# Kernel tuning notes

Measured on AMD Instinct MI355X. Metric: run time of the kernel, lower is better.

## Reference

```python
import jax, jax.numpy as jnp
import numpy as np

N = 100_000          # nodes
E = 1_600_000        # edges (avg degree 16)
IN_C, OUT_C = 256, 128


def setup_inputs() -> dict:
    key = jax.random.key(0)
    k1, k2, k3, k4, k5 = jax.random.split(key, 5)
    X = jax.random.normal(k1, (N, IN_C), dtype=jnp.float32)
    # nn.Linear(in, out, bias=False) weight has shape [out, in]
    W = jax.random.normal(k2, (OUT_C, IN_C), dtype=jnp.float32) * (1.0 / np.sqrt(IN_C))
    A_rows = jnp.sort(jax.random.randint(k3, (E,), 0, N, dtype=jnp.int32))
    A_cols = jax.random.randint(k4, (E,), 0, N, dtype=jnp.int32)
    # positive values mimicking symmetric-normalized adjacency entries
    A_vals = jax.random.uniform(k5, (E,), dtype=jnp.float32) * (1.0 / 16.0)
    return {"X": X, "W": W, "A_rows": A_rows, "A_cols": A_cols, "A_vals": A_vals}


def reference(X, W, A_rows, A_cols, A_vals):
    # X = self._linear(X)  ->  X @ W^T   [N, OUT_C]
    H = jnp.einsum("ni,oi->no", X, W)
    # X = torch.sparse.mm(A_hat, X): out[r] += v * H[c] for each edge (r, c, v)
    msgs = A_vals[:, None] * H[A_cols]                      # [E, OUT_C]
    out = jax.ops.segment_sum(msgs, A_rows, num_segments=N)  # [N, OUT_C]
    return out
```

## Files before the change

kernel.cpp:

```cpp
#include <hip/hip_runtime.h>
#include <hip/hip_bf16.h>

#define NNODES 100000
#define NEDGES 1600000
#define IN_C   256
#define OUT_C  128

typedef short bf16x8 __attribute__((ext_vector_type(8)));
typedef float f32x4  __attribute__((ext_vector_type(4)));

static __device__ __forceinline__ unsigned short f2bf(float f) {
    union { float f; unsigned u; } c; c.f = f;
    unsigned r = c.u + 0x7fffu + ((c.u >> 16) & 1u);
    return (unsigned short)(r >> 16);
}

union BF8 { bf16x8 v; unsigned short s[8]; };

__global__ __launch_bounds__(512, 4) void gemm_xwt(const float* __restrict__ X,
                                                   const float* __restrict__ W,
                                                   signed char* __restrict__ H8,
                                                   float* __restrict__ scale) {
    __shared__ unsigned short Wsh[128 * 256];

    const int tid  = threadIdx.x;
    const int lane = tid & 63;
    const int wid  = tid >> 6;

#pragma unroll
    for (int p = 0; p < 16; ++p) {
        int idx = p * 512 + tid;
        int n   = idx >> 6;
        int c4  = idx & 63;
        float4 v = *(const float4*)(W + (size_t)n * IN_C + c4 * 4);
        int byte = (n * 512 + c4 * 8) ^ ((n & 7) << 4);
        *(ushort4*)((char*)Wsh + byte) =
            make_ushort4(f2bf(v.x), f2bf(v.y), f2bf(v.z), f2bf(v.w));
    }
    __syncthreads();

    const int r0   = blockIdx.x * 128 + wid * 16;
    int arow = r0 + (lane & 15);
    if (arow > NNODES - 1) arow = NNODES - 1;
    const float* xrow = X + (size_t)arow * IN_C + (lane >> 4) * 8;

    f32x4 acc[8] = {};
#pragma unroll
    for (int ks = 0; ks < 8; ++ks) {
        float4 a0 = *(const float4*)(xrow + ks * 32);
        float4 a1 = *(const float4*)(xrow + ks * 32 + 4);
        BF8 t;
        t.s[0] = f2bf(a0.x); t.s[1] = f2bf(a0.y); t.s[2] = f2bf(a0.z); t.s[3] = f2bf(a0.w);
        t.s[4] = f2bf(a1.x); t.s[5] = f2bf(a1.y); t.s[6] = f2bf(a1.z); t.s[7] = f2bf(a1.w);
        const int kb = ks * 64 + (lane >> 4) * 16;
#pragma unroll
        for (int n8 = 0; n8 < 8; ++n8) {
            int nr   = n8 * 16 + (lane & 15);
            int byte = (nr * 512 + kb) ^ ((nr & 7) << 4);
            bf16x8 b = *(const bf16x8*)((const char*)Wsh + byte);
            acc[n8] = __builtin_amdgcn_mfma_f32_16x16x32_bf16(t.v, b, acc[n8],
                                                              0, 0, 0);
        }
    }

    float amax[4];
#pragma unroll
    for (int r = 0; r < 4; ++r) {
        float m = 0.f;
#pragma unroll
        for (int n8 = 0; n8 < 8; ++n8) m = fmaxf(m, fabsf(acc[n8][r]));
        amax[r] = m;
    }
#pragma unroll
    for (int d = 1; d < 16; d <<= 1)
#pragma unroll
        for (int r = 0; r < 4; ++r)
            amax[r] = fmaxf(amax[r], __shfl_xor(amax[r], d));

#pragma unroll
    for (int r = 0; r < 4; ++r) {
        int grow = r0 + (lane >> 4) * 4 + r;
        if (grow < NNODES) {
            float am  = amax[r];
            float inv = am > 0.f ? 127.f / am : 0.f;
            if ((lane & 15) == 0) scale[grow] = am * (1.f / 127.f);
#pragma unroll
            for (int n8 = 0; n8 < 8; ++n8) {
                float q = rintf(acc[n8][r] * inv);
                q = fminf(127.f, fmaxf(-127.f, q));
                H8[(size_t)grow * OUT_C + n8 * 16 + (lane & 15)] = (signed char)q;
            }
        }
    }
}

__global__ __launch_bounds__(256) void build_rowptr(const int* __restrict__ rows,
                                                    int* __restrict__ rowptr) {
    int r = blockIdx.x * 256 + threadIdx.x;
    if (r > NNODES) return;
    int lo = 0, hi = NEDGES;
    while (lo < hi) {
        int mid = (lo + hi) >> 1;
        if (rows[mid] < r) lo = mid + 1; else hi = mid;
    }
    rowptr[r] = lo;
}

static __device__ __forceinline__ void edge4(float acc[8], int ec, float ev,
                                             int jg, const uint2* __restrict__ H2,
                                             int cg) {
    int   c = __shfl(ec, jg);
    float v = __shfl(ev, jg);
    uint2 u = H2[(size_t)c * 16 + cg];
    acc[0] += v * (float)(signed char)(u.x);
    acc[1] += v * (float)(signed char)(u.x >> 8);
    acc[2] += v * (float)(signed char)(u.x >> 16);
    acc[3] += v * (float)(signed char)(u.x >> 24);
    acc[4] += v * (float)(signed char)(u.y);
    acc[5] += v * (float)(signed char)(u.y >> 8);
    acc[6] += v * (float)(signed char)(u.y >> 16);
    acc[7] += v * (float)(signed char)(u.y >> 24);
}

__global__ __launch_bounds__(256) void spmm_rows(const uint2* __restrict__ H2,
                                                 const int* __restrict__ rowptr,
                                                 const int* __restrict__ cols,
                                                 const float* __restrict__ vals,
                                                 const float* __restrict__ scale,
                                                 float* __restrict__ out) {
    const int wid  = threadIdx.x >> 6;
    const int lane = threadIdx.x & 63;
    const int g    = lane >> 4;
    const int cg   = lane & 15;

    const int rowA = (blockIdx.x * 4 + wid) * 2;
    const int sA = rowptr[rowA];
    const int eA = rowptr[rowA + 1];
    const int eB = rowptr[rowA + 2];

    float accA[8], accB[8];
#pragma unroll
    for (int t = 0; t < 8; ++t) { accA[t] = 0.f; accB[t] = 0.f; }

    int baseA = sA, baseB = eA;
    while (baseA < eA || baseB < eB) {
        int cntA = eA - baseA; cntA = cntA < 0 ? 0 : (cntA > 64 ? 64 : cntA);
        int cntB = eB - baseB; cntB = cntB < 0 ? 0 : (cntB > 64 ? 64 : cntB);

        int   ecA = 0, ecB = 0;
        float evA = 0.f, evB = 0.f;
        if (lane < cntA) { ecA = cols[baseA + lane]; evA = vals[baseA + lane] * scale[ecA]; }
        if (lane < cntB) { ecB = cols[baseB + lane]; evB = vals[baseB + lane] * scale[ecB]; }

        const int mx = cntA > cntB ? cntA : cntB;
        for (int j = 0; j < mx; j += 8) {
            if (j < cntA)     edge4(accA, ecA, evA, j + g,     H2, cg);
            if (j < cntB)     edge4(accB, ecB, evB, j + g,     H2, cg);
            if (j + 4 < cntA) edge4(accA, ecA, evA, j + 4 + g, H2, cg);
            if (j + 4 < cntB) edge4(accB, ecB, evB, j + 4 + g, H2, cg);
        }

        baseA += cntA;
        baseB += cntB;
    }

#pragma unroll
    for (int t = 0; t < 8; ++t) {
        accA[t] += __shfl_xor(accA[t], 16);
        accA[t] += __shfl_xor(accA[t], 32);
        accB[t] += __shfl_xor(accB[t], 16);
        accB[t] += __shfl_xor(accB[t], 32);
    }
    if (lane < 16) {
        f32x4 a0 = { accA[0], accA[1], accA[2], accA[3] };
        f32x4 a1 = { accA[4], accA[5], accA[6], accA[7] };
        f32x4 b0 = { accB[0], accB[1], accB[2], accB[3] };
        f32x4 b1 = { accB[4], accB[5], accB[6], accB[7] };
        __builtin_nontemporal_store(a0, (f32x4*)(out + (size_t)rowA * OUT_C + cg * 8));
        __builtin_nontemporal_store(a1, (f32x4*)(out + (size_t)rowA * OUT_C + cg * 8 + 4));
        __builtin_nontemporal_store(b0, (f32x4*)(out + (size_t)(rowA + 1) * OUT_C + cg * 8));
        __builtin_nontemporal_store(b1, (f32x4*)(out + (size_t)(rowA + 1) * OUT_C + cg * 8 + 4));
    }
}

extern "C" void kernel_launch(void* const* d_in, const int* in_sizes, int n_in,
                              void* d_out, int out_size, void* d_ws, size_t ws_size,
                              hipStream_t stream) {
    const float* X      = (const float*)d_in[0];
    const float* W      = (const float*)d_in[1];
    const int*   A_rows = (const int*)d_in[2];
    const int*   A_cols = (const int*)d_in[3];
    const float* A_vals = (const float*)d_in[4];
    float* out = (float*)d_out;

    signed char* H8    = (signed char*)d_ws;
    float*       scale = (float*)((char*)d_ws + (size_t)NNODES * OUT_C);
    int*         rowptr = (int*)((char*)scale + (size_t)NNODES * sizeof(float));

    gemm_xwt<<<(NNODES + 127) / 128, 512, 0, stream>>>(X, W, H8, scale);
    build_rowptr<<<(NNODES + 1 + 255) / 256, 256, 0, stream>>>(A_rows, rowptr);
    spmm_rows<<<(NNODES + 7) / 8, 256, 0, stream>>>((const uint2*)H8, rowptr,
                                                    A_cols, A_vals, scale, out);
}
```

Baseline: 91.87 us.

## Store H as offset uint8 and batch gathered loads ahead of FMAs

Quantized H is now stored as unsigned bytes with a +128 offset, so unpacking uses a plain byte-to-float conversion without sign extension. The offset is removed by tracking the per-row sum of edge weights and subtracting 128 times that sum at the end. The SpMM inner loop now handles 16 edges per step and issues all eight gathered loads before the FMAs, giving more memory-level parallelism. The cost is more live registers and extra float error from subtracting a large bias term.

```diff
diff --git a/kernel.cpp b/kernel.cpp
--- a/kernel.cpp
+++ b/kernel.cpp
@@ -19,7 +19,7 @@
 
 __global__ __launch_bounds__(512, 4) void gemm_xwt(const float* __restrict__ X,
                                                    const float* __restrict__ W,
-                                                   signed char* __restrict__ H8,
+                                                   unsigned char* __restrict__ H8,
                                                    float* __restrict__ scale) {
     __shared__ unsigned short Wsh[128 * 256];
 
@@ -88,7 +88,8 @@
             for (int n8 = 0; n8 < 8; ++n8) {
                 float q = rintf(acc[n8][r] * inv);
                 q = fminf(127.f, fmaxf(-127.f, q));
-                H8[(size_t)grow * OUT_C + n8 * 16 + (lane & 15)] = (signed char)q;
+                H8[(size_t)grow * OUT_C + n8 * 16 + (lane & 15)] =
+                    (unsigned char)((int)q + 128);
             }
         }
     }
@@ -106,20 +107,17 @@
     rowptr[r] = lo;
 }
 
-static __device__ __forceinline__ void edge4(float acc[8], int ec, float ev,
-                                             int jg, const uint2* __restrict__ H2,
-                                             int cg) {
-    int   c = __shfl(ec, jg);
-    float v = __shfl(ev, jg);
-    uint2 u = H2[(size_t)c * 16 + cg];
-    acc[0] += v * (float)(signed char)(u.x);
-    acc[1] += v * (float)(signed char)(u.x >> 8);
-    acc[2] += v * (float)(signed char)(u.x >> 16);
-    acc[3] += v * (float)(signed char)(u.x >> 24);
-    acc[4] += v * (float)(signed char)(u.y);
-    acc[5] += v * (float)(signed char)(u.y >> 8);
-    acc[6] += v * (float)(signed char)(u.y >> 16);
-    acc[7] += v * (float)(signed char)(u.y >> 24);
+static __device__ __forceinline__ void fma8(float acc[8], float* sw,
+                                            uint2 u, float v) {
+    *sw += v;
+    acc[0] += v * (float)( u.x        & 0xffu);
+    acc[1] += v * (float)((u.x >>  8) & 0xffu);
+    acc[2] += v * (float)((u.x >> 16) & 0xffu);
+    acc[3] += v * (float)( u.x >> 24);
+    acc[4] += v * (float)( u.y        & 0xffu);
+    acc[5] += v * (float)((u.y >>  8) & 0xffu);
+    acc[6] += v * (float)((u.y >> 16) & 0xffu);
+    acc[7] += v * (float)( u.y >> 24);
 }
 
 __global__ __launch_bounds__(256) void spmm_rows(const uint2* __restrict__ H2,
@@ -141,6 +139,7 @@
     float accA[8], accB[8];
 #pragma unroll
     for (int t = 0; t < 8; ++t) { accA[t] = 0.f; accB[t] = 0.f; }
+    float swA = 0.f, swB = 0.f;
 
     int baseA = sA, baseB = eA;
     while (baseA < eA || baseB < eB) {
@@ -153,11 +152,34 @@
         if (lane < cntB) { ecB = cols[baseB + lane]; evB = vals[baseB + lane] * scale[ecB]; }
 
         const int mx = cntA > cntB ? cntA : cntB;
-        for (int j = 0; j < mx; j += 8) {
-            if (j < cntA)     edge4(accA, ecA, evA, j + g,     H2, cg);
-            if (j < cntB)     edge4(accB, ecB, evB, j + g,     H2, cg);
-            if (j + 4 < cntA) edge4(accA, ecA, evA, j + 4 + g, H2, cg);
-            if (j + 4 < cntB) edge4(accB, ecB, evB, j + 4 + g, H2, cg);
+        for (int j = 0; j < mx; j += 16) {
+            const bool dA0 = j      < cntA, dA1 = j +  4 < cntA,
+                       dA2 = j + 8  < cntA, dA3 = j + 12 < cntA;
+            const bool dB0 = j      < cntB, dB1 = j +  4 < cntB,
+                       dB2 = j + 8  < cntB, dB3 = j + 12 < cntB;
+
+            int cA0 = __shfl(ecA, j + g),      cB0 = __shfl(ecB, j + g);
+            int cA1 = __shfl(ecA, j + 4 + g),  cB1 = __shfl(ecB, j + 4 + g);
+            int cA2 = __shfl(ecA, j + 8 + g),  cB2 = __shfl(ecB, j + 8 + g);
+            int cA3 = __shfl(ecA, j + 12 + g), cB3 = __shfl(ecB, j + 12 + g);
+            uint2 uA0, uA1, uA2, uA3, uB0, uB1, uB2, uB3;
+            if (dA0) uA0 = H2[(size_t)cA0 * 16 + cg];
+            if (dB0) uB0 = H2[(size_t)cB0 * 16 + cg];
+            if (dA1) uA1 = H2[(size_t)cA1 * 16 + cg];
+            if (dB1) uB1 = H2[(size_t)cB1 * 16 + cg];
+            if (dA2) uA2 = H2[(size_t)cA2 * 16 + cg];
+            if (dB2) uB2 = H2[(size_t)cB2 * 16 + cg];
+            if (dA3) uA3 = H2[(size_t)cA3 * 16 + cg];
+            if (dB3) uB3 = H2[(size_t)cB3 * 16 + cg];
+
+            if (dA0) fma8(accA, &swA, uA0, __shfl(evA, j + g));
+            if (dB0) fma8(accB, &swB, uB0, __shfl(evB, j + g));
+            if (dA1) fma8(accA, &swA, uA1, __shfl(evA, j + 4 + g));
+            if (dB1) fma8(accB, &swB, uB1, __shfl(evB, j + 4 + g));
+            if (dA2) fma8(accA, &swA, uA2, __shfl(evA, j + 8 + g));
+            if (dB2) fma8(accB, &swB, uB2, __shfl(evB, j + 8 + g));
+            if (dA3) fma8(accA, &swA, uA3, __shfl(evA, j + 12 + g));
+            if (dB3) fma8(accB, &swB, uB3, __shfl(evB, j + 12 + g));
         }
 
         baseA += cntA;
@@ -171,11 +193,15 @@
         accB[t] += __shfl_xor(accB[t], 16);
         accB[t] += __shfl_xor(accB[t], 32);
     }
+    swA += __shfl_xor(swA, 16); swA += __shfl_xor(swA, 32);
+    swB += __shfl_xor(swB, 16); swB += __shfl_xor(swB, 32);
+
     if (lane < 16) {
-        f32x4 a0 = { accA[0], accA[1], accA[2], accA[3] };
-        f32x4 a1 = { accA[4], accA[5], accA[6], accA[7] };
-        f32x4 b0 = { accB[0], accB[1], accB[2], accB[3] };
-        f32x4 b1 = { accB[4], accB[5], accB[6], accB[7] };
+        const float bA = 128.f * swA, bB = 128.f * swB;
+        f32x4 a0 = { accA[0] - bA, accA[1] - bA, accA[2] - bA, accA[3] - bA };
+        f32x4 a1 = { accA[4] - bA, accA[5] - bA, accA[6] - bA, accA[7] - bA };
+        f32x4 b0 = { accB[0] - bB, accB[1] - bB, accB[2] - bB, accB[3] - bB };
+        f32x4 b1 = { accB[4] - bB, accB[5] - bB, accB[6] - bB, accB[7] - bB };
         __builtin_nontemporal_store(a0, (f32x4*)(out + (size_t)rowA * OUT_C + cg * 8));
         __builtin_nontemporal_store(a1, (f32x4*)(out + (size_t)rowA * OUT_C + cg * 8 + 4));
         __builtin_nontemporal_store(b0, (f32x4*)(out + (size_t)(rowA + 1) * OUT_C + cg * 8));
@@ -193,9 +219,9 @@
     const float* A_vals = (const float*)d_in[4];
     float* out = (float*)d_out;
 
-    signed char* H8    = (signed char*)d_ws;
-    float*       scale = (float*)((char*)d_ws + (size_t)NNODES * OUT_C);
-    int*         rowptr = (int*)((char*)scale + (size_t)NNODES * sizeof(float));
+    unsigned char* H8    = (unsigned char*)d_ws;
+    float*         scale = (float*)((char*)d_ws + (size_t)NNODES * OUT_C);
+    int*           rowptr = (int*)((char*)scale + (size_t)NNODES * sizeof(float));
 
     gemm_xwt<<<(NNODES + 127) / 128, 512, 0, stream>>>(X, W, H8, scale);
     build_rowptr<<<(NNODES + 1 + 255) / 256, 256, 0, stream>>>(A_rows, rowptr);
```

Result: slower. 94.86 us (+3.2%).

## Store H as biased uint8 and gather 16 bytes per lane in SpMM

Applied to the files above, without the earlier changes.

The GEMM now writes quantized H as unsigned bytes offset by 128. The SpMM converts them with plain unsigned byte extracts instead of sign-extending, and removes the bias at the end by subtracting 128 times the sum of edge weights. Each lane now loads a uint4 (16 channels) instead of a uint2, and all gathers in an iteration are issued before the FMAs to increase memory-level parallelism. In exchange each lane holds twice as many accumulators, the reduction gains an extra shuffle stage, and subtracting the bias may cost a little fp32 accuracy.

```diff
diff --git a/kernel.cpp b/kernel.cpp
--- a/kernel.cpp
+++ b/kernel.cpp
@@ -19,7 +19,7 @@
 
 __global__ __launch_bounds__(512, 4) void gemm_xwt(const float* __restrict__ X,
                                                    const float* __restrict__ W,
-                                                   signed char* __restrict__ H8,
+                                                   unsigned char* __restrict__ H8,
                                                    float* __restrict__ scale) {
     __shared__ unsigned short Wsh[128 * 256];
 
@@ -88,7 +88,8 @@
             for (int n8 = 0; n8 < 8; ++n8) {
                 float q = rintf(acc[n8][r] * inv);
                 q = fminf(127.f, fmaxf(-127.f, q));
-                H8[(size_t)grow * OUT_C + n8 * 16 + (lane & 15)] = (signed char)q;
+                H8[(size_t)grow * OUT_C + n8 * 16 + (lane & 15)] =
+                    (unsigned char)((int)q + 128);
             }
         }
     }
@@ -106,23 +107,20 @@
     rowptr[r] = lo;
 }
 
-static __device__ __forceinline__ void edge4(float acc[8], int ec, float ev,
-                                             int jg, const uint2* __restrict__ H2,
-                                             int cg) {
-    int   c = __shfl(ec, jg);
-    float v = __shfl(ev, jg);
-    uint2 u = H2[(size_t)c * 16 + cg];
-    acc[0] += v * (float)(signed char)(u.x);
-    acc[1] += v * (float)(signed char)(u.x >> 8);
-    acc[2] += v * (float)(signed char)(u.x >> 16);
-    acc[3] += v * (float)(signed char)(u.x >> 24);
-    acc[4] += v * (float)(signed char)(u.y);
-    acc[5] += v * (float)(signed char)(u.y >> 8);
-    acc[6] += v * (float)(signed char)(u.y >> 16);
-    acc[7] += v * (float)(signed char)(u.y >> 24);
-}
-
-__global__ __launch_bounds__(256) void spmm_rows(const uint2* __restrict__ H2,
+static __device__ __forceinline__ void fma16(float acc[16], float* sw,
+                                             uint4 u, float v) {
+    *sw += v;
+#pragma unroll
+    for (int d = 0; d < 4; ++d) {
+        unsigned ud = (&u.x)[d];
+        acc[d * 4 + 0] += v * (float)( ud        & 0xffu);
+        acc[d * 4 + 1] += v * (float)((ud >>  8) & 0xffu);
+        acc[d * 4 + 2] += v * (float)((ud >> 16) & 0xffu);
+        acc[d * 4 + 3] += v * (float)( ud >> 24);
+    }
+}
+
+__global__ __launch_bounds__(256) void spmm_rows(const uint4* __restrict__ H4,
                                                  const int* __restrict__ rowptr,
                                                  const int* __restrict__ cols,
                                                  const float* __restrict__ vals,
@@ -130,17 +128,18 @@
                                                  float* __restrict__ out) {
     const int wid  = threadIdx.x >> 6;
     const int lane = threadIdx.x & 63;
-    const int g    = lane >> 4;
-    const int cg   = lane & 15;
+    const int g    = lane >> 3;
+    const int cg   = lane & 7;
 
     const int rowA = (blockIdx.x * 4 + wid) * 2;
     const int sA = rowptr[rowA];
     const int eA = rowptr[rowA + 1];
     const int eB = rowptr[rowA + 2];
 
-    float accA[8], accB[8];
-#pragma unroll
-    for (int t = 0; t < 8; ++t) { accA[t] = 0.f; accB[t] = 0.f; }
+    float accA[16], accB[16];
+#pragma unroll
+    for (int t = 0; t < 16; ++t) { accA[t] = 0.f; accB[t] = 0.f; }
+    float swA = 0.f, swB = 0.f;
 
     int baseA = sA, baseB = eA;
     while (baseA < eA || baseB < eB) {
@@ -153,11 +152,24 @@
         if (lane < cntB) { ecB = cols[baseB + lane]; evB = vals[baseB + lane] * scale[ecB]; }
 
         const int mx = cntA > cntB ? cntA : cntB;
-        for (int j = 0; j < mx; j += 8) {
-            if (j < cntA)     edge4(accA, ecA, evA, j + g,     H2, cg);
-            if (j < cntB)     edge4(accB, ecB, evB, j + g,     H2, cg);
-            if (j + 4 < cntA) edge4(accA, ecA, evA, j + 4 + g, H2, cg);
-            if (j + 4 < cntB) edge4(accB, ecB, evB, j + 4 + g, H2, cg);
+        for (int j = 0; j < mx; j += 16) {
+            const bool dA0 = j < cntA, dA1 = j + 8 < cntA;
+            const bool dB0 = j < cntB, dB1 = j + 8 < cntB;
+
+            uint4 uA0, uA1, uB0, uB1;
+            float vA0, vA1, vB0, vB1;
+            if (dA0) { int c = __shfl(ecA, j + g);     vA0 = __shfl(evA, j + g);
+                       uA0 = H4[(size_t)c * 8 + cg]; }
+            if (dB0) { int c = __shfl(ecB, j + g);     vB0 = __shfl(evB, j + g);
+                       uB0 = H4[(size_t)c * 8 + cg]; }
+            if (dA1) { int c = __shfl(ecA, j + 8 + g); vA1 = __shfl(evA, j + 8 + g);
+                       uA1 = H4[(size_t)c * 8 + cg]; }
+            if (dB1) { int c = __shfl(ecB, j + 8 + g); vB1 = __shfl(evB, j + 8 + g);
+                       uB1 = H4[(size_t)c * 8 + cg]; }
+            if (dA0) fma16(accA, &swA, uA0, vA0);
+            if (dB0) fma16(accB, &swB, uB0, vB0);
+            if (dA1) fma16(accA, &swA, uA1, vA1);
+            if (dB1) fma16(accB, &swB, uB1, vB1);
         }
 
         baseA += cntA;
@@ -165,21 +177,30 @@
     }
 
 #pragma unroll
-    for (int t = 0; t < 8; ++t) {
+    for (int t = 0; t < 16; ++t) {
+        accA[t] += __shfl_xor(accA[t], 8);
         accA[t] += __shfl_xor(accA[t], 16);
         accA[t] += __shfl_xor(accA[t], 32);
+        accB[t] += __shfl_xor(accB[t], 8);
         accB[t] += __shfl_xor(accB[t], 16);
         accB[t] += __shfl_xor(accB[t], 32);
     }
-    if (lane < 16) {
-        f32x4 a0 = { accA[0], accA[1], accA[2], accA[3] };
-        f32x4 a1 = { accA[4], accA[5], accA[6], accA[7] };
-        f32x4 b0 = { accB[0], accB[1], accB[2], accB[3] };
-        f32x4 b1 = { accB[4], accB[5], accB[6], accB[7] };
-        __builtin_nontemporal_store(a0, (f32x4*)(out + (size_t)rowA * OUT_C + cg * 8));
-        __builtin_nontemporal_store(a1, (f32x4*)(out + (size_t)rowA * OUT_C + cg * 8 + 4));
-        __builtin_nontemporal_store(b0, (f32x4*)(out + (size_t)(rowA + 1) * OUT_C + cg * 8));
-        __builtin_nontemporal_store(b1, (f32x4*)(out + (size_t)(rowA + 1) * OUT_C + cg * 8 + 4));
+    swA += __shfl_xor(swA, 8); swA += __shfl_xor(swA, 16); swA += __shfl_xor(swA, 32);
+    swB += __shfl_xor(swB, 8); swB += __shfl_xor(swB, 16); swB += __shfl_xor(swB, 32);
+
+    if (lane < 8) {
+        const float bA = 128.f * swA, bB = 128.f * swB;
+        float* oA = out + (size_t)rowA * OUT_C + cg * 16;
+        float* oB = out + (size_t)(rowA + 1) * OUT_C + cg * 16;
+#pragma unroll
+        for (int q = 0; q < 4; ++q) {
+            f32x4 va = { accA[q * 4 + 0] - bA, accA[q * 4 + 1] - bA,
+                         accA[q * 4 + 2] - bA, accA[q * 4 + 3] - bA };
+            f32x4 vb = { accB[q * 4 + 0] - bB, accB[q * 4 + 1] - bB,
+                         accB[q * 4 + 2] - bB, accB[q * 4 + 3] - bB };
+            __builtin_nontemporal_store(va, (f32x4*)(oA + q * 4));
+            __builtin_nontemporal_store(vb, (f32x4*)(oB + q * 4));
+        }
     }
 }
 
@@ -193,12 +214,12 @@
     const float* A_vals = (const float*)d_in[4];
     float* out = (float*)d_out;
 
-    signed char* H8    = (signed char*)d_ws;
-    float*       scale = (float*)((char*)d_ws + (size_t)NNODES * OUT_C);
-    int*         rowptr = (int*)((char*)scale + (size_t)NNODES * sizeof(float));
+    unsigned char* H8    = (unsigned char*)d_ws;
+    float*         scale = (float*)((char*)d_ws + (size_t)NNODES * OUT_C);
+    int*           rowptr = (int*)((char*)scale + (size_t)NNODES * sizeof(float));
 
     gemm_xwt<<<(NNODES + 127) / 128, 512, 0, stream>>>(X, W, H8, scale);
     build_rowptr<<<(NNODES + 1 + 255) / 256, 256, 0, stream>>>(A_rows, rowptr);
-    spmm_rows<<<(NNODES + 7) / 8, 256, 0, stream>>>((const uint2*)H8, rowptr,
+    spmm_rows<<<(NNODES + 7) / 8, 256, 0, stream>>>((const uint4*)H8, rowptr,
                                                     A_cols, A_vals, scale, out);
 }
```

Measured after the change: 105.9 us. +15.2%, slower.

## Use offset-binary int8 H, nontemporal gathers, and persistent grid-stride SpMM

Applied to the files above, without the earlier changes.

The int8 features are now stored offset by 128 as unsigned bytes, so the SpMM can unpack them with masks and shifts instead of sign extension, and it removes the bias afterwards using a per-row running sum of edge weights. The H gathers switch to nontemporal loads. The SpMM launches a fixed grid of 2048 blocks that stride over row pairs instead of one wave per row pair. Together these aim to trim unpack ALU work and launch/tail overhead. In exchange they add a per-edge weight sum and a subtraction, and the nontemporal hint on the random gathers may hurt cache reuse of H rows.

```diff
diff --git a/kernel.cpp b/kernel.cpp
--- a/kernel.cpp
+++ b/kernel.cpp
@@ -8,6 +8,7 @@
 
 typedef short bf16x8 __attribute__((ext_vector_type(8)));
 typedef float f32x4  __attribute__((ext_vector_type(4)));
+typedef unsigned int u32x2 __attribute__((ext_vector_type(2)));
 
 static __device__ __forceinline__ unsigned short f2bf(float f) {
     union { float f; unsigned u; } c; c.f = f;
@@ -19,7 +20,7 @@
 
 __global__ __launch_bounds__(512, 4) void gemm_xwt(const float* __restrict__ X,
                                                    const float* __restrict__ W,
-                                                   signed char* __restrict__ H8,
+                                                   unsigned char* __restrict__ H8,
                                                    float* __restrict__ scale) {
     __shared__ unsigned short Wsh[128 * 256];
 
@@ -88,7 +89,8 @@
             for (int n8 = 0; n8 < 8; ++n8) {
                 float q = rintf(acc[n8][r] * inv);
                 q = fminf(127.f, fmaxf(-127.f, q));
-                H8[(size_t)grow * OUT_C + n8 * 16 + (lane & 15)] = (signed char)q;
+                H8[(size_t)grow * OUT_C + n8 * 16 + (lane & 15)] =
+                    (unsigned char)((int)q + 128);
             }
         }
     }
@@ -106,23 +108,27 @@
     rowptr[r] = lo;
 }
 
-static __device__ __forceinline__ void edge4(float acc[8], int ec, float ev,
-                                             int jg, const uint2* __restrict__ H2,
-                                             int cg) {
+#define SPMM_BLOCKS 2048
+
+static __device__ __forceinline__ void edge4nt(float acc[8], float* sw,
+                                               int ec, float ev, int jg,
+                                               const u32x2* __restrict__ H2,
+                                               int cg) {
     int   c = __shfl(ec, jg);
     float v = __shfl(ev, jg);
-    uint2 u = H2[(size_t)c * 16 + cg];
-    acc[0] += v * (float)(signed char)(u.x);
-    acc[1] += v * (float)(signed char)(u.x >> 8);
-    acc[2] += v * (float)(signed char)(u.x >> 16);
-    acc[3] += v * (float)(signed char)(u.x >> 24);
-    acc[4] += v * (float)(signed char)(u.y);
-    acc[5] += v * (float)(signed char)(u.y >> 8);
-    acc[6] += v * (float)(signed char)(u.y >> 16);
-    acc[7] += v * (float)(signed char)(u.y >> 24);
-}
-
-__global__ __launch_bounds__(256) void spmm_rows(const uint2* __restrict__ H2,
+    u32x2 u = __builtin_nontemporal_load(H2 + (size_t)c * 16 + cg);
+    *sw += v;
+    acc[0] += v * (float)( u[0]        & 0xffu);
+    acc[1] += v * (float)((u[0] >>  8) & 0xffu);
+    acc[2] += v * (float)((u[0] >> 16) & 0xffu);
+    acc[3] += v * (float)( u[0] >> 24);
+    acc[4] += v * (float)( u[1]        & 0xffu);
+    acc[5] += v * (float)((u[1] >>  8) & 0xffu);
+    acc[6] += v * (float)((u[1] >> 16) & 0xffu);
+    acc[7] += v * (float)( u[1] >> 24);
+}
+
+__global__ __launch_bounds__(256) void spmm_rows(const u32x2* __restrict__ H2,
                                                  const int* __restrict__ rowptr,
                                                  const int* __restrict__ cols,
                                                  const float* __restrict__ vals,
@@ -133,53 +139,63 @@
     const int g    = lane >> 4;
     const int cg   = lane & 15;
 
-    const int rowA = (blockIdx.x * 4 + wid) * 2;
-    const int sA = rowptr[rowA];
-    const int eA = rowptr[rowA + 1];
-    const int eB = rowptr[rowA + 2];
-
-    float accA[8], accB[8];
-#pragma unroll
-    for (int t = 0; t < 8; ++t) { accA[t] = 0.f; accB[t] = 0.f; }
-
-    int baseA = sA, baseB = eA;
-    while (baseA < eA || baseB < eB) {
-        int cntA = eA - baseA; cntA = cntA < 0 ? 0 : (cntA > 64 ? 64 : cntA);
-        int cntB = eB - baseB; cntB = cntB < 0 ? 0 : (cntB > 64 ? 64 : cntB);
-
-        int   ecA = 0, ecB = 0;
-        float evA = 0.f, evB = 0.f;
-        if (lane < cntA) { ecA = cols[baseA + lane]; evA = vals[baseA + lane] * scale[ecA]; }
-        if (lane < cntB) { ecB = cols[baseB + lane]; evB = vals[baseB + lane] * scale[ecB]; }
-
-        const int mx = cntA > cntB ? cntA : cntB;
-        for (int j = 0; j < mx; j += 8) {
-            if (j < cntA)     edge4(accA, ecA, evA, j + g,     H2, cg);
-            if (j < cntB)     edge4(accB, ecB, evB, j + g,     H2, cg);
-            if (j + 4 < cntA) edge4(accA, ecA, evA, j + 4 + g, H2, cg);
-            if (j + 4 < cntB) edge4(accB, ecB, evB, j + 4 + g, H2, cg);
-        }
-
-        baseA += cntA;
-        baseB += cntB;
-    }
-
-#pragma unroll
-    for (int t = 0; t < 8; ++t) {
-        accA[t] += __shfl_xor(accA[t], 16);
-        accA[t] += __shfl_xor(accA[t], 32);
-        accB[t] += __shfl_xor(accB[t], 16);
-        accB[t] += __shfl_xor(accB[t], 32);
-    }
-    if (lane < 16) {
-        f32x4 a0 = { accA[0], accA[1], accA[2], accA[3] };
-        f32x4 a1 = { accA[4], accA[5], accA[6], accA[7] };
-        f32x4 b0 = { accB[0], accB[1], accB[2], accB[3] };
-        f32x4 b1 = { accB[4], accB[5], accB[6], accB[7] };
-        __builtin_nontemporal_store(a0, (f32x4*)(out + (size_t)rowA * OUT_C + cg * 8));
-        __builtin_nontemporal_store(a1, (f32x4*)(out + (size_t)rowA * OUT_C + cg * 8 + 4));
-        __builtin_nontemporal_store(b0, (f32x4*)(out + (size_t)(rowA + 1) * OUT_C + cg * 8));
-        __builtin_nontemporal_store(b1, (f32x4*)(out + (size_t)(rowA + 1) * OUT_C + cg * 8 + 4));
+    for (int pair = blockIdx.x * 4 + wid; pair < NNODES / 2;
+         pair += SPMM_BLOCKS * 4) {
+        const int rowA = pair * 2;
+        const int sA = rowptr[rowA];
+        const int eA = rowptr[rowA + 1];
+        const int eB = rowptr[rowA + 2];
+
+        float accA[8], accB[8];
+#pragma unroll
+        for (int t = 0; t < 8; ++t) { accA[t] = 0.f; accB[t] = 0.f; }
+        float swA = 0.f, swB = 0.f;
+
+        int baseA = sA, baseB = eA;
+        while (baseA < eA || baseB < eB) {
+            int cntA = eA - baseA; cntA = cntA < 0 ? 0 : (cntA > 64 ? 64 : cntA);
+            int cntB = eB - baseB; cntB = cntB < 0 ? 0 : (cntB > 64 ? 64 : cntB);
+
+            int   ecA = 0, ecB = 0;
+            float evA = 0.f, evB = 0.f;
+            if (lane < cntA) { ecA = cols[baseA + lane];
+                               evA = vals[baseA + lane] * scale[ecA]; }
+            if (lane < cntB) { ecB = cols[baseB + lane];
+                               evB = vals[baseB + lane] * scale[ecB]; }
+
+            const int mx = cntA > cntB ? cntA : cntB;
+            for (int j = 0; j < mx; j += 8) {
+                if (j < cntA)     edge4nt(accA, &swA, ecA, evA, j + g,     H2, cg);
+                if (j < cntB)     edge4nt(accB, &swB, ecB, evB, j + g,     H2, cg);
+                if (j + 4 < cntA) edge4nt(accA, &swA, ecA, evA, j + 4 + g, H2, cg);
+                if (j + 4 < cntB) edge4nt(accB, &swB, ecB, evB, j + 4 + g, H2, cg);
+            }
+
+            baseA += cntA;
+            baseB += cntB;
+        }
+
+#pragma unroll
+        for (int t = 0; t < 8; ++t) {
+            accA[t] += __shfl_xor(accA[t], 16);
+            accA[t] += __shfl_xor(accA[t], 32);
+            accB[t] += __shfl_xor(accB[t], 16);
+            accB[t] += __shfl_xor(accB[t], 32);
+        }
+        swA += __shfl_xor(swA, 16); swA += __shfl_xor(swA, 32);
+        swB += __shfl_xor(swB, 16); swB += __shfl_xor(swB, 32);
+
+        if (lane < 16) {
+            const float bA = 128.f * swA, bB = 128.f * swB;
+            f32x4 a0 = { accA[0] - bA, accA[1] - bA, accA[2] - bA, accA[3] - bA };
+            f32x4 a1 = { accA[4] - bA, accA[5] - bA, accA[6] - bA, accA[7] - bA };
+            f32x4 b0 = { accB[0] - bB, accB[1] - bB, accB[2] - bB, accB[3] - bB };
+            f32x4 b1 = { accB[4] - bB, accB[5] - bB, accB[6] - bB, accB[7] - bB };
+            __builtin_nontemporal_store(a0, (f32x4*)(out + (size_t)rowA * OUT_C + cg * 8));
+            __builtin_nontemporal_store(a1, (f32x4*)(out + (size_t)rowA * OUT_C + cg * 8 + 4));
+            __builtin_nontemporal_store(b0, (f32x4*)(out + (size_t)(rowA + 1) * OUT_C + cg * 8));
+            __builtin_nontemporal_store(b1, (f32x4*)(out + (size_t)(rowA + 1) * OUT_C + cg * 8 + 4));
+        }
     }
 }
 
@@ -193,12 +209,12 @@
     const float* A_vals = (const float*)d_in[4];
     float* out = (float*)d_out;
 
-    signed char* H8    = (signed char*)d_ws;
-    float*       scale = (float*)((char*)d_ws + (size_t)NNODES * OUT_C);
-    int*         rowptr = (int*)((char*)scale + (size_t)NNODES * sizeof(float));
+    unsigned char* H8     = (unsigned char*)d_ws;
+    float*         scale  = (float*)((char*)d_ws + (size_t)NNODES * OUT_C);
+    int*           rowptr = (int*)((char*)scale + (size_t)NNODES * sizeof(float));
 
     gemm_xwt<<<(NNODES + 127) / 128, 512, 0, stream>>>(X, W, H8, scale);
     build_rowptr<<<(NNODES + 1 + 255) / 256, 256, 0, stream>>>(A_rows, rowptr);
-    spmm_rows<<<(NNODES + 7) / 8, 256, 0, stream>>>((const uint2*)H8, rowptr,
-                                                    A_cols, A_vals, scale, out);
-}
+    spmm_rows<<<SPMM_BLOCKS, 256, 0, stream>>>((const u32x2*)H8, rowptr,
+                                               A_cols, A_vals, scale, out);
+}
```

Result: slower. 111.8 us (+21.7%).
